# Performance work log

Hardware: AMD Instinct MI355X
Metric: run time of the kernel (lower is better)

The kernel has to match this reference:

```python
import jax, jax.numpy as jnp
import numpy as np

N, D, M, E, K = 16384, 512, 1024, 8, 2
LOSS_COEF = 0.01
EPS = 1e-10


def setup_inputs() -> dict:
    key = jax.random.key(0)
    ks = jax.random.split(key, 6)
    x = jax.random.normal(ks[0], (N, D), dtype=jnp.float32)
    # gate weight (torch init is zeros; use small random so routing is non-degenerate)
    w_gate = 0.02 * jax.random.normal(ks[1], (D, E), dtype=jnp.float32)
    # stacked expert FFN params: Linear(D->M), GELU, Linear(M->D)
    W1 = jax.random.normal(ks[2], (E, D, M), dtype=jnp.float32) / np.sqrt(D)
    b1 = jnp.zeros((E, M), dtype=jnp.float32)
    W2 = jax.random.normal(ks[3], (E, M, D), dtype=jnp.float32) / np.sqrt(M)
    b2 = jnp.zeros((E, D), dtype=jnp.float32)
    return {"x": x, "w_gate": w_gate, "W1": W1, "b1": b1, "W2": W2, "b2": b2}


def _cv_squared(v):
    # torch .var() is unbiased (ddof=1)
    v = v.astype(jnp.float32)
    return jnp.var(v, ddof=1) / (jnp.mean(v) ** 2 + EPS)


def reference(x, w_gate, W1, b1, W2, b2):
    n = x.shape[0]
    # --- noisy_top_k_gating (eval path: no noise) ---
    logits = x @ w_gate                                  # [N, E]
    top_logits, top_idx = jax.lax.top_k(logits, min(K + 1, E))
    topk_logits = top_logits[:, :K]                      # [N, K]
    topk_idx = top_idx[:, :K]                            # [N, K]
    topk_gates = jax.nn.softmax(topk_logits, axis=-1)    # [N, K]
    gates = jnp.zeros_like(logits).at[jnp.arange(n)[:, None], topk_idx].set(topk_gates)
    importance = gates.sum(axis=0)                       # [E]
    load = (gates > 0).sum(axis=0).astype(jnp.float32)   # [E]
    loss = LOSS_COEF * (_cv_squared(importance) + _cv_squared(load))
    # --- experts (dense equivalent of sparse dispatch/combine: gate==0 rows contribute 0) ---
    h = jnp.einsum('nd,edm->enm', x, W1) + b1[:, None, :]     # [E, N, M]
    h = jax.nn.gelu(h, approximate=False)
    out = jnp.einsum('enm,emd->end', h, W2) + b2[:, None, :]  # [E, N, D]
    y = jnp.einsum('ne,end->nd', gates, out)                  # [N, D]
    return (y, loss)
```

## Files before the change

kernel.cpp:

```cpp
#include <hip/hip_runtime.h>
#include <math.h>

#define NTOK 16384
#define DDIM 512
#define MDIM 1024
#define NEXP 8
#define TMAX 264

typedef __attribute__((ext_vector_type(8))) short short8;
typedef __attribute__((ext_vector_type(4))) float floatx4;

__device__ inline unsigned short f2bf(float f){
  union { float f; unsigned int u; } v; v.f = f;
  unsigned int u = v.u;
  u += ((u >> 16) & 1u) + 0x7fffu;
  return (unsigned short)(u >> 16);
}

__device__ inline float bf2f(unsigned short s){
  union { unsigned int u; float f; } v;
  v.u = ((unsigned int)s) << 16;
  return v.f;
}

__device__ inline float gelu_fast(float x){
  float u = x * 0.70710678118654752f;
  float a = fabsf(u);
  float t = __builtin_amdgcn_rcpf(fmaf(0.3275911f, a, 1.0f));
  float p = fmaf(1.061405429f, t, -1.453152027f);
  p = fmaf(p, t, 1.421413741f);
  p = fmaf(p, t, -0.284496736f);
  p = fmaf(p, t, 0.254829592f);
  p = p * t;
  float e = __expf(-u * u);
  float erfa = fmaf(-p, e, 1.0f);
  float erfu = copysignf(erfa, u);
  return 0.5f * x * (1.0f + erfu);
}

__device__ __forceinline__ void gload16(const unsigned short* g, unsigned short* l){
  __builtin_amdgcn_global_load_lds(
      (const __attribute__((address_space(1))) void*)g,
      (__attribute__((address_space(3))) void*)l,
      16, 0, 0);
}


__global__ void init_small_kernel(int* counts, float* imp){
  int t = threadIdx.x;
  if (t < NEXP){ counts[t] = 0; imp[t] = 0.0f; }
}

__global__ void transpose_conv_kernel(const float* __restrict__ in,
                                      unsigned short* __restrict__ out,
                                      int R, int C){
  __shared__ float tile[32][33];
  int e  = blockIdx.z;
  int c0 = blockIdx.x << 5;
  int r0 = blockIdx.y << 5;
  const float* src = in + (size_t)e * R * C;
  unsigned short* dst = out + (size_t)e * R * C;
  int tc = threadIdx.x;
  int tr = threadIdx.y;
  #pragma unroll
  for (int i = 0; i < 32; i += 8)
    tile[tr + i][tc] = src[(size_t)(r0 + tr + i) * C + c0 + tc];
  __syncthreads();
  #pragma unroll
  for (int i = 0; i < 32; i += 8)
    dst[(size_t)(c0 + tr + i) * R + r0 + tc] = f2bf(tile[tc][tr + i]);
}


__global__ __launch_bounds__(256)
void gating_kernel(const float* __restrict__ x,
                   const float* __restrict__ wg,
                   unsigned short* __restrict__ xb,
                   int* __restrict__ tok_e, float* __restrict__ tok_g,
                   int* __restrict__ counts, float* __restrict__ imp){
  __shared__ int   lcnt[NEXP];
  __shared__ float limp[NEXP];
  int t = threadIdx.x;
  if (t < NEXP){ lcnt[t] = 0; limp[t] = 0.0f; }
  __syncthreads();

  int wave = t >> 6;
  int lane = t & 63;

  for (int it = 0; it < 16; it++){
    int n = blockIdx.x * 64 + it * 4 + wave;

    const float4* xp = (const float4*)(x + (size_t)n * DDIM + lane * 8);
    float4 a = xp[0], b = xp[1];
    float xv[8] = {a.x, a.y, a.z, a.w, b.x, b.y, b.z, b.w};

    short8 xo;
    #pragma unroll
    for (int j = 0; j < 8; j++) xo[j] = (short)f2bf(xv[j]);
    *(short8*)(xb + (size_t)n * DDIM + lane * 8) = xo;

    double acc[NEXP];
    #pragma unroll
    for (int e = 0; e < NEXP; e++) acc[e] = 0.0;
    #pragma unroll
    for (int j = 0; j < 8; j++){
      const float* wr = wg + (size_t)(lane * 8 + j) * NEXP;
      #pragma unroll
      for (int e = 0; e < NEXP; e++) acc[e] += (double)xv[j] * (double)wr[e];
    }
    #pragma unroll
    for (int off = 32; off >= 1; off >>= 1){
      #pragma unroll
      for (int e = 0; e < NEXP; e++) acc[e] += __shfl_xor(acc[e], off);
    }
    if (lane == 0){
      int i0 = -1, i1 = -1;
      double l0 = -1e300, l1 = -1e300;
      #pragma unroll
      for (int e = 0; e < NEXP; e++){
        double v = acc[e];
        if (v > l0){ l1 = l0; i1 = i0; l0 = v; i0 = e; }
        else if (v > l1){ l1 = v; i1 = e; }
      }
      float ex = expf((float)(l1 - l0));
      float g0 = 1.0f / (1.0f + ex);
      float g1 = ex / (1.0f + ex);
      tok_e[n * 2]     = i0; tok_e[n * 2 + 1] = i1;
      tok_g[n * 2]     = g0; tok_g[n * 2 + 1] = g1;
      atomicAdd(&lcnt[i0], 1); atomicAdd(&lcnt[i1], 1);
      atomicAdd(&limp[i0], g0); atomicAdd(&limp[i1], g1);
    }
  }
  __syncthreads();
  if (t < NEXP){
    atomicAdd(&counts[t], lcnt[t]);
    atomicAdd(&imp[t], limp[t]);
  }
}

__global__ void loss_scan_kernel(const int* __restrict__ counts,
                                 const float* __restrict__ imp,
                                 int* __restrict__ offsets, int* __restrict__ cursor,
                                 int* __restrict__ tile_pre,
                                 float* __restrict__ out_loss){
  int off = 0, tp = 0;
  double si = 0, si2 = 0, sl = 0, sl2 = 0;
  for (int e = 0; e < NEXP; e++){
    offsets[e] = off; cursor[e] = off;
    tile_pre[e] = tp;
    tp += (counts[e] + 127) >> 7;
    off += counts[e];
    double im = (double)imp[e];
    double ld = (double)counts[e];
    si += im; si2 += im * im;
    sl += ld; sl2 += ld * ld;
  }
  offsets[NEXP] = off;
  tile_pre[NEXP] = tp;
  double mi = si / 8.0, ml = sl / 8.0;
  double vi = (si2 - 8.0 * mi * mi) / 7.0;
  double vl = (sl2 - 8.0 * ml * ml) / 7.0;
  double loss = 0.01 * (vi / (mi * mi + 1e-10) + vl / (ml * ml + 1e-10));
  *out_loss = (float)loss;
}

__global__ __launch_bounds__(256)
void scatter_kernel(const int* __restrict__ tok_e,
                    int* __restrict__ cursor,
                    int* __restrict__ btok, int* __restrict__ slot_of){
  __shared__ int lcnt[NEXP];
  __shared__ int lbase[NEXP];
  int t = threadIdx.x;
  if (t < NEXP) lcnt[t] = 0;
  __syncthreads();

  int n = blockIdx.x * 256 + t;
  int e0 = tok_e[n * 2], e1 = tok_e[n * 2 + 1];
  int r0 = atomicAdd(&lcnt[e0], 1);
  int r1 = atomicAdd(&lcnt[e1], 1);
  __syncthreads();
  if (t < NEXP) lbase[t] = atomicAdd(&cursor[t], lcnt[t]);
  __syncthreads();
  int s0 = lbase[e0] + r0;
  int s1 = lbase[e1] + r1;
  btok[s0] = n;
  btok[s1] = n;
  slot_of[n * 2]     = s0;
  slot_of[n * 2 + 1] = s1;
}


__global__ __launch_bounds__(256)
void gemm1_kernel(const unsigned short* __restrict__ xb,
                  const unsigned short* __restrict__ w1t,
                  const float* __restrict__ b1,
                  const int* __restrict__ offsets,
                  const int* __restrict__ tile_pre,
                  const int* __restrict__ btok,
                  unsigned short* __restrict__ H){
  int ct = blockIdx.x / TMAX;
  int tt = blockIdx.x % TMAX;
  if (tt >= tile_pre[NEXP]) return;
  int e = 0;
  while (tt >= tile_pre[e + 1]) e++;
  int rt = tt - tile_pre[e];
  int off = offsets[e];
  int cnt = offsets[e + 1] - off;
  int r0 = rt << 7;

  __shared__ unsigned short As[2][128 * 32];
  __shared__ unsigned short Bs[2][128 * 32];

  int t = threadIdx.x;
  int srow = t >> 2;
  int scol = (t & 3) << 3;
  int w = t >> 6;

  int ra0 = r0 + srow;        if (ra0 >= cnt) ra0 = cnt - 1;
  int ra1 = r0 + 64 + srow;   if (ra1 >= cnt) ra1 = cnt - 1;
  const unsigned short* aptr0 = xb + (size_t)btok[off + ra0] * DDIM + scol;
  const unsigned short* aptr1 = xb + (size_t)btok[off + ra1] * DDIM + scol;
  const unsigned short* bptr0 = w1t + ((size_t)e * MDIM + (ct << 7) + srow) * DDIM + scol;
  const unsigned short* bptr1 = bptr0 + (size_t)64 * DDIM;

  int lane = t & 63;
  int wr = (w >> 1) << 6;
  int wc = (w & 1) << 6;
  int lm = lane & 15;
  int lq = lane >> 4;

  gload16(aptr0, &As[0][w * 512]);
  gload16(aptr1, &As[0][2048 + w * 512]);
  gload16(bptr0, &Bs[0][w * 512]);
  gload16(bptr1, &Bs[0][2048 + w * 512]);

  floatx4 acc[4][4] = {};
  int p = 0;
  #pragma unroll 4
  for (int ki = 0; ki < DDIM / 32; ki++){
    __syncthreads();
    if (ki + 1 < DDIM / 32){
      int k0 = (ki + 1) * 32;
      gload16(aptr0 + k0, &As[p ^ 1][w * 512]);
      gload16(aptr1 + k0, &As[p ^ 1][2048 + w * 512]);
      gload16(bptr0 + k0, &Bs[p ^ 1][w * 512]);
      gload16(bptr1 + k0, &Bs[p ^ 1][2048 + w * 512]);
    }
    short8 af[4], bf[4];
    #pragma unroll
    for (int i = 0; i < 4; i++) af[i] = *(const short8*)&As[p][(wr + i * 16 + lm) * 32 + lq * 8];
    #pragma unroll
    for (int j = 0; j < 4; j++) bf[j] = *(const short8*)&Bs[p][(wc + j * 16 + lm) * 32 + lq * 8];
    #pragma unroll
    for (int i = 0; i < 4; i++)
      #pragma unroll
      for (int j = 0; j < 4; j++)
        acc[i][j] = __builtin_amdgcn_mfma_f32_16x16x32_bf16(bf[j], af[i], acc[i][j], 0, 0, 0);
    p ^= 1;
  }

  const float* bias = b1 + e * MDIM + (ct << 7) + wc;
  #pragma unroll
  for (int i = 0; i < 4; i++){
    int tokl = r0 + wr + i * 16 + lm;
    bool valid = tokl < cnt;
    unsigned short* hrow = H + (size_t)(off + (valid ? tokl : 0)) * MDIM + (ct << 7) + wc;
    #pragma unroll
    for (int j = 0; j < 4; j++){
      float4 bv = *(const float4*)(bias + j * 16 + lq * 4);
      float g0 = gelu_fast(acc[i][j][0] + bv.x);
      float g1 = gelu_fast(acc[i][j][1] + bv.y);
      float g2 = gelu_fast(acc[i][j][2] + bv.z);
      float g3 = gelu_fast(acc[i][j][3] + bv.w);
      uint2 pk;
      pk.x = (unsigned)f2bf(g0) | ((unsigned)f2bf(g1) << 16);
      pk.y = (unsigned)f2bf(g2) | ((unsigned)f2bf(g3) << 16);
      if (valid) *(uint2*)(hrow + j * 16 + lq * 4) = pk;
    }
  }
}

__global__ __launch_bounds__(256)
void gemm2_kernel(const unsigned short* __restrict__ H,
                  const unsigned short* __restrict__ w2t,
                  const float* __restrict__ b2,
                  const int* __restrict__ offsets,
                  const int* __restrict__ tile_pre,
                  unsigned short* __restrict__ O){
  int ct = blockIdx.x / TMAX;
  int tt = blockIdx.x % TMAX;
  if (tt >= tile_pre[NEXP]) return;
  int e = 0;
  while (tt >= tile_pre[e + 1]) e++;
  int rt = tt - tile_pre[e];
  int off = offsets[e];
  int cnt = offsets[e + 1] - off;
  int r0 = rt << 7;

  __shared__ unsigned short As[2][128 * 32];
  __shared__ unsigned short Bs[2][128 * 32];

  int t = threadIdx.x;
  int srow = t >> 2;
  int scol = (t & 3) << 3;
  int w = t >> 6;

  int ra0 = r0 + srow;        if (ra0 >= cnt) ra0 = cnt - 1;
  int ra1 = r0 + 64 + srow;   if (ra1 >= cnt) ra1 = cnt - 1;
  const unsigned short* aptr0 = H + (size_t)(off + ra0) * MDIM + scol;
  const unsigned short* aptr1 = H + (size_t)(off + ra1) * MDIM + scol;
  const unsigned short* bptr0 = w2t + ((size_t)e * DDIM + (ct << 7) + srow) * MDIM + scol;
  const unsigned short* bptr1 = bptr0 + (size_t)64 * MDIM;

  int lane = t & 63;
  int wr = (w >> 1) << 6;
  int wc = (w & 1) << 6;
  int lm = lane & 15;
  int lq = lane >> 4;

  gload16(aptr0, &As[0][w * 512]);
  gload16(aptr1, &As[0][2048 + w * 512]);
  gload16(bptr0, &Bs[0][w * 512]);
  gload16(bptr1, &Bs[0][2048 + w * 512]);

  floatx4 acc[4][4] = {};
  int p = 0;
  #pragma unroll 4
  for (int ki = 0; ki < MDIM / 32; ki++){
    __syncthreads();
    if (ki + 1 < MDIM / 32){
      int k0 = (ki + 1) * 32;
      gload16(aptr0 + k0, &As[p ^ 1][w * 512]);
      gload16(aptr1 + k0, &As[p ^ 1][2048 + w * 512]);
      gload16(bptr0 + k0, &Bs[p ^ 1][w * 512]);
      gload16(bptr1 + k0, &Bs[p ^ 1][2048 + w * 512]);
    }
    short8 af[4], bf[4];
    #pragma unroll
    for (int i = 0; i < 4; i++) af[i] = *(const short8*)&As[p][(wr + i * 16 + lm) * 32 + lq * 8];
    #pragma unroll
    for (int j = 0; j < 4; j++) bf[j] = *(const short8*)&Bs[p][(wc + j * 16 + lm) * 32 + lq * 8];
    #pragma unroll
    for (int i = 0; i < 4; i++)
      #pragma unroll
      for (int j = 0; j < 4; j++)
        acc[i][j] = __builtin_amdgcn_mfma_f32_16x16x32_bf16(bf[j], af[i], acc[i][j], 0, 0, 0);
    p ^= 1;
  }

  const float* bias = b2 + e * DDIM + (ct << 7) + wc;
  #pragma unroll
  for (int i = 0; i < 4; i++){
    int tokl = r0 + wr + i * 16 + lm;
    bool valid = tokl < cnt;
    unsigned short* orow = O + (size_t)(off + (valid ? tokl : 0)) * DDIM + (ct << 7) + wc;
    #pragma unroll
    for (int j = 0; j < 4; j++){
      float4 bv = *(const float4*)(bias + j * 16 + lq * 4);
      uint2 pk;
      pk.x = (unsigned)f2bf(acc[i][j][0] + bv.x) | ((unsigned)f2bf(acc[i][j][1] + bv.y) << 16);
      pk.y = (unsigned)f2bf(acc[i][j][2] + bv.z) | ((unsigned)f2bf(acc[i][j][3] + bv.w) << 16);
      if (valid) *(uint2*)(orow + j * 16 + lq * 4) = pk;
    }
  }
}


__global__ __launch_bounds__(256)
void combine_kernel(const unsigned short* __restrict__ O,
                    const float* __restrict__ tok_g,
                    const int* __restrict__ slot_of,
                    float* __restrict__ y){
  int wave = threadIdx.x >> 6;
  int lane = threadIdx.x & 63;
  int n = blockIdx.x * 4 + wave;
  int s0 = slot_of[n * 2], s1 = slot_of[n * 2 + 1];
  float g0 = tok_g[n * 2], g1 = tok_g[n * 2 + 1];
  short8 a = *(const short8*)(O + (size_t)s0 * DDIM + lane * 8);
  short8 b = *(const short8*)(O + (size_t)s1 * DDIM + lane * 8);
  float4 o0, o1;
  float* po0 = (float*)&o0;
  float* po1 = (float*)&o1;
  #pragma unroll
  for (int j = 0; j < 4; j++){
    po0[j] = g0 * bf2f((unsigned short)a[j]) + g1 * bf2f((unsigned short)b[j]);
    po1[j] = g0 * bf2f((unsigned short)a[j + 4]) + g1 * bf2f((unsigned short)b[j + 4]);
  }
  float4* yp = (float4*)(y + (size_t)n * DDIM + lane * 8);
  yp[0] = o0;
  yp[1] = o1;
}


extern "C" void kernel_launch(void* const* d_in, const int* in_sizes, int n_in,
                              void* d_out, int out_size, void* d_ws, size_t ws_size,
                              hipStream_t stream){
  const float* x  = (const float*)d_in[0];
  const float* wg = (const float*)d_in[1];
  const float* W1 = (const float*)d_in[2];
  const float* b1 = (const float*)d_in[3];
  const float* W2 = (const float*)d_in[4];
  const float* b2 = (const float*)d_in[5];
  float* y = (float*)d_out;

  char* ws = (char*)d_ws;
  size_t o = 0;
  auto alloc = [&](size_t bytes)->char*{
    char* p = ws + o;
    o += (bytes + 255) & ~(size_t)255;
    return p;
  };
  unsigned short* xb   = (unsigned short*)alloc((size_t)NTOK * DDIM * 2);
  unsigned short* w1t  = (unsigned short*)alloc((size_t)NEXP * MDIM * DDIM * 2);
  unsigned short* w2t  = (unsigned short*)alloc((size_t)NEXP * DDIM * MDIM * 2);
  unsigned short* H    = (unsigned short*)alloc((size_t)NTOK * 2 * MDIM * 2);
  unsigned short* O    = (unsigned short*)alloc((size_t)NTOK * 2 * DDIM * 2);
  int*   btok    = (int*)  alloc((size_t)NTOK * 2 * 4);
  int*   slot_of = (int*)  alloc((size_t)NTOK * 2 * 4);
  int*   tok_e   = (int*)  alloc((size_t)NTOK * 2 * 4);
  float* tok_g   = (float*)alloc((size_t)NTOK * 2 * 4);
  int*   counts  = (int*)  alloc(64);
  float* imp     = (float*)alloc(64);
  int*   offsets = (int*)  alloc(64);
  int*   cursor  = (int*)  alloc(64);
  int*   tile_pre= (int*)  alloc(64);

  hipLaunchKernelGGL(init_small_kernel, dim3(1), dim3(64), 0, stream, counts, imp);
  hipLaunchKernelGGL(transpose_conv_kernel, dim3(MDIM / 32, DDIM / 32, NEXP), dim3(32, 8), 0, stream,
                     W1, w1t, DDIM, MDIM);
  hipLaunchKernelGGL(transpose_conv_kernel, dim3(DDIM / 32, MDIM / 32, NEXP), dim3(32, 8), 0, stream,
                     W2, w2t, MDIM, DDIM);
  hipLaunchKernelGGL(gating_kernel, dim3(NTOK / 64), dim3(256), 0, stream,
                     x, wg, xb, tok_e, tok_g, counts, imp);
  hipLaunchKernelGGL(loss_scan_kernel, dim3(1), dim3(1), 0, stream,
                     counts, imp, offsets, cursor, tile_pre, y + (size_t)NTOK * DDIM);
  hipLaunchKernelGGL(scatter_kernel, dim3(NTOK / 256), dim3(256), 0, stream,
                     tok_e, cursor, btok, slot_of);
  hipLaunchKernelGGL(gemm1_kernel, dim3(TMAX * 8), dim3(256), 0, stream,
                     xb, w1t, b1, offsets, tile_pre, btok, H);
  hipLaunchKernelGGL(gemm2_kernel, dim3(TMAX * 4), dim3(256), 0, stream,
                     H, w2t, b2, offsets, tile_pre, O);
  hipLaunchKernelGGL(combine_kernel, dim3(NTOK / 4), dim3(256), 0, stream,
                     O, tok_g, slot_of, y);
}
```

Baseline: 332.8 us.

## Single-buffer GEMM LDS tiles and fold counter init into transpose kernel

Both expert GEMM kernels drop the double-buffered LDS prefetch and switch to a single buffer: load a tile, barrier, compute, barrier. This halves shared memory per block, which may let more blocks fit per CU, but it gives up overlap of global loads with MFMA work inside a block. Separately, the tiny init kernel that zeroes counts and importance is merged into the first transpose launch to save one kernel launch.

```diff
diff --git a/kernel.cpp b/kernel.cpp
--- a/kernel.cpp
+++ b/kernel.cpp
@@ -46,14 +46,14 @@
 }
 
 
-__global__ void init_small_kernel(int* counts, float* imp){
-  int t = threadIdx.x;
-  if (t < NEXP){ counts[t] = 0; imp[t] = 0.0f; }
-}
-
 __global__ void transpose_conv_kernel(const float* __restrict__ in,
                                       unsigned short* __restrict__ out,
-                                      int R, int C){
+                                      int R, int C,
+                                      int* counts, float* imp, int doinit){
+  if (doinit && blockIdx.x == 0 && blockIdx.y == 0 && blockIdx.z == 0 &&
+      threadIdx.y == 0 && threadIdx.x < NEXP){
+    counts[threadIdx.x] = 0; imp[threadIdx.x] = 0.0f;
+  }
   __shared__ float tile[32][33];
   int e  = blockIdx.z;
   int c0 = blockIdx.x << 5;
@@ -208,8 +208,8 @@
   int cnt = offsets[e + 1] - off;
   int r0 = rt << 7;
 
-  __shared__ unsigned short As[2][128 * 32];
-  __shared__ unsigned short Bs[2][128 * 32];
+  __shared__ unsigned short As[128 * 32];
+  __shared__ unsigned short Bs[128 * 32];
 
   int t = threadIdx.x;
   int srow = t >> 2;
@@ -223,40 +223,35 @@
   const unsigned short* bptr0 = w1t + ((size_t)e * MDIM + (ct << 7) + srow) * DDIM + scol;
   const unsigned short* bptr1 = bptr0 + (size_t)64 * DDIM;
 
+  unsigned short* As0 = As + w * 512;
+  unsigned short* As1 = As + 2048 + w * 512;
+  unsigned short* Bs0 = Bs + w * 512;
+  unsigned short* Bs1 = Bs + 2048 + w * 512;
+
   int lane = t & 63;
   int wr = (w >> 1) << 6;
   int wc = (w & 1) << 6;
   int lm = lane & 15;
   int lq = lane >> 4;
 
-  gload16(aptr0, &As[0][w * 512]);
-  gload16(aptr1, &As[0][2048 + w * 512]);
-  gload16(bptr0, &Bs[0][w * 512]);
-  gload16(bptr1, &Bs[0][2048 + w * 512]);
-
   floatx4 acc[4][4] = {};
-  int p = 0;
-  #pragma unroll 4
-  for (int ki = 0; ki < DDIM / 32; ki++){
+  for (int k0 = 0; k0 < DDIM; k0 += 32){
+    gload16(aptr0 + k0, As0);
+    gload16(aptr1 + k0, As1);
+    gload16(bptr0 + k0, Bs0);
+    gload16(bptr1 + k0, Bs1);
     __syncthreads();
-    if (ki + 1 < DDIM / 32){
-      int k0 = (ki + 1) * 32;
-      gload16(aptr0 + k0, &As[p ^ 1][w * 512]);
-      gload16(aptr1 + k0, &As[p ^ 1][2048 + w * 512]);
-      gload16(bptr0 + k0, &Bs[p ^ 1][w * 512]);
-      gload16(bptr1 + k0, &Bs[p ^ 1][2048 + w * 512]);
-    }
     short8 af[4], bf[4];
     #pragma unroll
-    for (int i = 0; i < 4; i++) af[i] = *(const short8*)&As[p][(wr + i * 16 + lm) * 32 + lq * 8];
-    #pragma unroll
-    for (int j = 0; j < 4; j++) bf[j] = *(const short8*)&Bs[p][(wc + j * 16 + lm) * 32 + lq * 8];
+    for (int i = 0; i < 4; i++) af[i] = *(const short8*)&As[(wr + i * 16 + lm) * 32 + lq * 8];
+    #pragma unroll
+    for (int j = 0; j < 4; j++) bf[j] = *(const short8*)&Bs[(wc + j * 16 + lm) * 32 + lq * 8];
     #pragma unroll
     for (int i = 0; i < 4; i++)
       #pragma unroll
       for (int j = 0; j < 4; j++)
         acc[i][j] = __builtin_amdgcn_mfma_f32_16x16x32_bf16(bf[j], af[i], acc[i][j], 0, 0, 0);
-    p ^= 1;
+    __syncthreads();
   }
 
   const float* bias = b1 + e * MDIM + (ct << 7) + wc;
@@ -297,8 +292,8 @@
   int cnt = offsets[e + 1] - off;
   int r0 = rt << 7;
 
-  __shared__ unsigned short As[2][128 * 32];
-  __shared__ unsigned short Bs[2][128 * 32];
+  __shared__ unsigned short As[128 * 32];
+  __shared__ unsigned short Bs[128 * 32];
 
   int t = threadIdx.x;
   int srow = t >> 2;
@@ -312,40 +307,35 @@
   const unsigned short* bptr0 = w2t + ((size_t)e * DDIM + (ct << 7) + srow) * MDIM + scol;
   const unsigned short* bptr1 = bptr0 + (size_t)64 * MDIM;
 
+  unsigned short* As0 = As + w * 512;
+  unsigned short* As1 = As + 2048 + w * 512;
+  unsigned short* Bs0 = Bs + w * 512;
+  unsigned short* Bs1 = Bs + 2048 + w * 512;
+
   int lane = t & 63;
   int wr = (w >> 1) << 6;
   int wc = (w & 1) << 6;
   int lm = lane & 15;
   int lq = lane >> 4;
 
-  gload16(aptr0, &As[0][w * 512]);
-  gload16(aptr1, &As[0][2048 + w * 512]);
-  gload16(bptr0, &Bs[0][w * 512]);
-  gload16(bptr1, &Bs[0][2048 + w * 512]);
-
   floatx4 acc[4][4] = {};
-  int p = 0;
-  #pragma unroll 4
-  for (int ki = 0; ki < MDIM / 32; ki++){
+  for (int k0 = 0; k0 < MDIM; k0 += 32){
+    gload16(aptr0 + k0, As0);
+    gload16(aptr1 + k0, As1);
+    gload16(bptr0 + k0, Bs0);
+    gload16(bptr1 + k0, Bs1);
     __syncthreads();
-    if (ki + 1 < MDIM / 32){
-      int k0 = (ki + 1) * 32;
-      gload16(aptr0 + k0, &As[p ^ 1][w * 512]);
-      gload16(aptr1 + k0, &As[p ^ 1][2048 + w * 512]);
-      gload16(bptr0 + k0, &Bs[p ^ 1][w * 512]);
-      gload16(bptr1 + k0, &Bs[p ^ 1][2048 + w * 512]);
-    }
     short8 af[4], bf[4];
     #pragma unroll
-    for (int i = 0; i < 4; i++) af[i] = *(const short8*)&As[p][(wr + i * 16 + lm) * 32 + lq * 8];
-    #pragma unroll
-    for (int j = 0; j < 4; j++) bf[j] = *(const short8*)&Bs[p][(wc + j * 16 + lm) * 32 + lq * 8];
+    for (int i = 0; i < 4; i++) af[i] = *(const short8*)&As[(wr + i * 16 + lm) * 32 + lq * 8];
+    #pragma unroll
+    for (int j = 0; j < 4; j++) bf[j] = *(const short8*)&Bs[(wc + j * 16 + lm) * 32 + lq * 8];
     #pragma unroll
     for (int i = 0; i < 4; i++)
       #pragma unroll
       for (int j = 0; j < 4; j++)
         acc[i][j] = __builtin_amdgcn_mfma_f32_16x16x32_bf16(bf[j], af[i], acc[i][j], 0, 0, 0);
-    p ^= 1;
+    __syncthreads();
   }
 
   const float* bias = b2 + e * DDIM + (ct << 7) + wc;
@@ -425,11 +415,10 @@
   int*   cursor  = (int*)  alloc(64);
   int*   tile_pre= (int*)  alloc(64);
 
-  hipLaunchKernelGGL(init_small_kernel, dim3(1), dim3(64), 0, stream, counts, imp);
   hipLaunchKernelGGL(transpose_conv_kernel, dim3(MDIM / 32, DDIM / 32, NEXP), dim3(32, 8), 0, stream,
-                     W1, w1t, DDIM, MDIM);
+                     W1, w1t, DDIM, MDIM, counts, imp, 1);
   hipLaunchKernelGGL(transpose_conv_kernel, dim3(DDIM / 32, MDIM / 32, NEXP), dim3(32, 8), 0, stream,
-                     W2, w2t, MDIM, DDIM);
+                     W2, w2t, MDIM, DDIM, counts, imp, 0);
   hipLaunchKernelGGL(gating_kernel, dim3(NTOK / 64), dim3(256), 0, stream,
                      x, wg, xb, tok_e, tok_g, counts, imp);
   hipLaunchKernelGGL(loss_scan_kernel, dim3(1), dim3(1), 0, stream,
```

After: 312.9 us. 1.06x faster.
